# Kernel optimization log

Measured on AMD Instinct MI355X. Metric: run time of the kernel, lower is better.

Reference implementation:

```python
import jax, jax.numpy as jnp
import numpy as np

T, B, S, A, H = 512, 1024, 64, 16, 128  # timesteps, envs, state_dim, action_dim, LAYER_SIZE


def setup_inputs() -> dict:
    key = jax.random.key(0)
    ks = jax.random.split(key, 12)

    def w(k, shape, fan_in, std=1.0):
        return std * jax.random.normal(k, shape, jnp.float32) / jnp.sqrt(fan_in)

    x = jax.random.normal(ks[0], (T * B, S), jnp.float32)
    done = (jax.random.uniform(ks[1], (T * B,)) < 0.05).astype(jnp.float32)
    action = jax.random.randint(ks[2], (T * B,), 0, A, jnp.int32)
    gru_state = jnp.zeros((1, B, H), jnp.float32)

    return {
        "x": x, "done": done, "action": action, "gru_state": gru_state,
        "W1": w(ks[3], (H, S), S), "b1": jnp.zeros((H,), jnp.float32),
        "W2": w(ks[4], (H, H), H), "b2": jnp.zeros((H,), jnp.float32),
        "W_ih": w(ks[5], (3 * H, H), H), "b_ih": jnp.zeros((3 * H,), jnp.float32),
        "W_hh": w(ks[6], (3 * H, H), H), "b_hh": jnp.zeros((3 * H,), jnp.float32),
        "Wa": w(ks[7], (A, H), H, std=0.01), "ba": jnp.zeros((A,), jnp.float32),
        "Wc": w(ks[8], (1, H), H), "bc": jnp.zeros((1,), jnp.float32),
    }


def reference(x, done, action, gru_state, W1, b1, W2, b2, W_ih, b_ih, W_hh, b_hh, Wa, ba, Wc, bc):
    # MLP encoder: Linear->ReLU->Linear->ReLU  [T*B, H]
    h2 = jax.nn.relu(jax.nn.relu(x @ W1.T + b1) @ W2.T + b2)
    # Precompute input-side GRU gates for all timesteps: [T, B, 3H]
    gx = (h2 @ W_ih.T + b_ih).reshape(T, B, 3 * H)
    d = done.reshape(T, B)
    h0 = gru_state[0]  # [B, H]

    def step(h, inp):
        gx_t, d_t = inp
        h = (1.0 - d_t)[:, None] * h  # done-mask state reset
        gh = h @ W_hh.T + b_hh
        xr, xz, xn = jnp.split(gx_t, 3, axis=-1)
        hr, hz, hn = jnp.split(gh, 3, axis=-1)
        r = jax.nn.sigmoid(xr + hr)
        z = jax.nn.sigmoid(xz + hz)
        n = jnp.tanh(xn + r * hn)
        h_new = (1.0 - z) * n + z * h
        return h_new, h_new

    h_last, hs = jax.lax.scan(step, h0, (gx, d))
    hidden = hs.reshape(T * B, H)

    logits = hidden @ Wa.T + ba
    logp = jax.nn.log_softmax(logits, axis=-1)
    log_prob = jnp.take_along_axis(logp, action[:, None].astype(jnp.int32), axis=1)[:, 0]
    entropy = -jnp.sum(jnp.exp(logp) * logp, axis=-1)
    # DETACH=True: critic runs on detached hidden
    value = jax.lax.stop_gradient(hidden) @ Wc.T + bc  # [T*B, 1]

    main = jnp.concatenate([log_prob[:, None], entropy[:, None], value], axis=1)  # [T*B, 3]
    return main, h_last[None]
```

## Files before the change

kernel.cpp:

```cpp
#include <hip/hip_runtime.h>
#include <stdint.h>

#define TT 512
#define BB 1024
#define SS 64
#define HH 128
#define TBR (TT*BB)
#define NTILE (TBR/16)
#define MTPB 16
#define MGRID (NTILE/MTPB)

typedef __attribute__((ext_vector_type(8))) short short8;
typedef __attribute__((ext_vector_type(4))) float floatx4;
typedef unsigned short u16;
typedef unsigned int u32;
typedef struct { u32 x, y; } u32x2;

__device__ __forceinline__ float bf2f(u16 u){union{u32 i;float f;}v;v.i=((u32)u)<<16;return v.f;}
__device__ __forceinline__ u16 f2bf(float f){union{float f;u32 i;}v;v.f=f;u32 r=v.i+0x7FFFu+((v.i>>16)&1u);return (u16)(r>>16);}
__device__ __forceinline__ float frcp(float x){ return __builtin_amdgcn_rcpf(x); }

__device__ __forceinline__ bool buf_is_bf16(const u16* p) {
  int ok = 0;
#pragma unroll
  for (int i = 0; i < 32; ++i) {
    u32 v = p[2*i] & 0x7FFFu;
    u32 e = v >> 7;
    ok += (v == 0u || (e >= 96u && e <= 128u)) ? 1 : 0;
  }
  return ok >= 24;
}

template<bool BF> __device__ __forceinline__ float ld1(const void* p, size_t i){
  if constexpr (BF) return bf2f(((const u16*)p)[i]);
  else              return ((const float*)p)[i];
}
__device__ __forceinline__ short8 pack8(floatx4 a, floatx4 b){
  short8 r;
  r[0]=(short)f2bf(a[0]); r[1]=(short)f2bf(a[1]); r[2]=(short)f2bf(a[2]); r[3]=(short)f2bf(a[3]);
  r[4]=(short)f2bf(b[0]); r[5]=(short)f2bf(b[1]); r[6]=(short)f2bf(b[2]); r[7]=(short)f2bf(b[3]);
  return r;
}
template<bool BF> __device__ __forceinline__ short8 ld8(const void* p, size_t i){
  if constexpr (BF) return *(const short8*)((const u16*)p + i);
  else {
    const float* f = (const float*)p + i;
    return pack8(*(const floatx4*)f, *(const floatx4*)(f + 4));
  }
}
template<bool BF> __device__ __forceinline__ void st1(void* p, size_t i, float v){
  if constexpr (BF) ((u16*)p)[i] = f2bf(v);
  else              ((float*)p)[i] = v;
}

__device__ __forceinline__ void barrier_lds() {
  __asm__ __volatile__("" ::: "memory");
  __builtin_amdgcn_s_waitcnt(0xC07F);
  __builtin_amdgcn_s_barrier();
  __asm__ __volatile__("" ::: "memory");
}

__device__ __forceinline__ int fragidx(int m,int k){
  return ((k>>5)<<9)+((m+(((k>>3)&3)<<4))<<3)+(k&7);
}
__device__ __forceinline__ floatx4 mfma(short8 a, short8 b, floatx4 c){
  return __builtin_amdgcn_mfma_f32_16x16x32_bf16(a,b,c,0,0,0);
}

template<bool BF>
__global__ __launch_bounds__(512, 2) void k_mlp(
    const void* __restrict__ x,
    const void* __restrict__ W1, const void* __restrict__ b1,
    const void* __restrict__ W2, const void* __restrict__ b2,
    u16* __restrict__ h2g)
{
  if (buf_is_bf16((const u16*)W1) != BF) return;
  const int tid = threadIdx.x, lane = tid & 63, wv = tid >> 6;
  const int n16 = lane & 15, q = lane >> 4;
  const int jj = 16*wv + n16;

  __shared__ __align__(16) u16 h1f[2][2048];
  __shared__ __align__(16) u16 h2f[2][2048];

  short8 w1f[2], w2f[4];
  float b1v, b2v;
  {
#pragma unroll
    for (int ks = 0; ks < 2; ++ks) w1f[ks] = ld8<BF>(W1, (size_t)jj*SS + ks*32 + q*8);
    b1v = ld1<BF>(b1, jj);
#pragma unroll
    for (int ks = 0; ks < 4; ++ks) w2f[ks] = ld8<BF>(W2, (size_t)jj*HH + ks*32 + q*8);
    b2v = ld1<BF>(b2, jj);
  }

  const int tile0 = blockIdx.x * MTPB;

  short8 xb[2]; floatx4 xf[4];
  {
    size_t base = ((size_t)(tile0*16 + n16))*SS + q*8;
    if constexpr (BF) {
      xb[0] = *(const short8*)((const u16*)x + base);
      xb[1] = *(const short8*)((const u16*)x + base + 32);
    } else {
      const float* f = (const float*)x + base;
      xf[0] = *(const floatx4*)f;       xf[1] = *(const floatx4*)(f+4);
      xf[2] = *(const floatx4*)(f+32);  xf[3] = *(const floatx4*)(f+36);
    }
  }

  for (int i = 0; i < MTPB + 2; ++i) {
    short8 xc0, xc1;
    if (i < MTPB) {
      if constexpr (BF) { xc0 = xb[0]; xc1 = xb[1]; }
      else              { xc0 = pack8(xf[0], xf[1]); xc1 = pack8(xf[2], xf[3]); }
    }
    if (i + 1 < MTPB) {
      size_t base = ((size_t)((tile0+i+1)*16 + n16))*SS + q*8;
      if constexpr (BF) {
        xb[0] = *(const short8*)((const u16*)x + base);
        xb[1] = *(const short8*)((const u16*)x + base + 32);
      } else {
        const float* f = (const float*)x + base;
        xf[0] = *(const floatx4*)f;       xf[1] = *(const floatx4*)(f+4);
        xf[2] = *(const floatx4*)(f+32);  xf[3] = *(const floatx4*)(f+36);
      }
    }
    if (i < MTPB) {
      floatx4 a = {0.f,0.f,0.f,0.f};
      a = mfma(xc0, w1f[0], a);
      a = mfma(xc1, w1f[1], a);
#pragma unroll
      for (int r = 0; r < 4; ++r) {
        float v = a[r] + b1v; v = v > 0.f ? v : 0.f;
        h1f[i&1][fragidx(4*q + r, jj)] = f2bf(v);
      }
    }
    if (i >= 1 && i <= MTPB) {
      short8 h1a[4];
#pragma unroll
      for (int ks = 0; ks < 4; ++ks)
        h1a[ks] = *(const short8*)(&h1f[(i-1)&1][0] + ks*512 + lane*8);
      floatx4 a = {0.f,0.f,0.f,0.f};
#pragma unroll
      for (int ks = 0; ks < 4; ++ks) a = mfma(h1a[ks], w2f[ks], a);
#pragma unroll
      for (int r = 0; r < 4; ++r) {
        float v = a[r] + b2v; v = v > 0.f ? v : 0.f;
        h2f[(i-1)&1][fragidx(4*q + r, jj)] = f2bf(v);
      }
    }
    if (i >= 2) {
      const int td = tile0 + i - 2;
      u32x2 v2 = *(const u32x2*)(&h2f[i&1][tid*4]);
      *(u32x2*)(h2g + (size_t)td*2048 + tid*4) = v2;
    }
    barrier_lds();
  }
}

template<bool BF>
__global__ __launch_bounds__(512, 2) void k_scan_split(
    const void* __restrict__ done_, const void* __restrict__ gstate,
    const void* __restrict__ Wih, const void* __restrict__ bih,
    const void* __restrict__ Whh, const void* __restrict__ bhh,
    const void* __restrict__ Wa, const void* __restrict__ ba,
    const void* __restrict__ Wc, const void* __restrict__ bc,
    const void* __restrict__ W1,
    const u16* __restrict__ h2g,
    float* __restrict__ lgws, float* __restrict__ vws,
    void* __restrict__ out)
{
  if (buf_is_bf16((const u16*)W1) != BF) return;

  const int tid = threadIdx.x, lane = tid & 63, wv = tid >> 6;
  const int n16 = lane & 15, q = lane >> 4;
  const int b0 = blockIdx.x * 16, bx = blockIdx.x;
  const int jj = 16*wv + n16;

  __shared__ __align__(16) u16 hbuf[2][2048];

  short8 wif[3][4], whf[3][4], scf[4];
  float bihv2, bhv2, bb0, bb1;
  {
    float bi0, bi1, bh0, bh1;
#pragma unroll
    for (int g = 0; g < 3; ++g) {
      int grow = g*128 + jj;
#pragma unroll
      for (int ks = 0; ks < 4; ++ks) {
        wif[g][ks] = ld8<BF>(Wih, (size_t)grow*HH + ks*32 + q*8);
        whf[g][ks] = ld8<BF>(Whh, (size_t)grow*HH + ks*32 + q*8);
      }
      float bi = ld1<BF>(bih, grow), bh = ld1<BF>(bhh, grow);
      if (g == 0) { bi0 = bi; bh0 = bh; }
      else if (g == 1) { bi1 = bi; bh1 = bh; }
      else { bihv2 = bi; bhv2 = bh; }
    }
    bb0 = bi0 + bh0;
    bb1 = bi1 + bh1;
  }
  if (wv == 1) {
#pragma unroll
    for (int ks = 0; ks < 4; ++ks) scf[ks] = ld8<BF>(Wa, (size_t)n16*HH + ks*32 + q*8);
  } else if (wv == 2) {
#pragma unroll
    for (int ks = 0; ks < 4; ++ks) {
      short8 z = {0,0,0,0,0,0,0,0};
      if (n16 == 0) z = ld8<BF>(Wc, (size_t)ks*32 + q*8);
      scf[ks] = z;
    }
  } else {
#pragma unroll
    for (int ks = 0; ks < 4; ++ks) { short8 z = {0,0,0,0,0,0,0,0}; scf[ks] = z; }
  }
  const float bav = ld1<BF>(ba, n16);
  const float bcv = ld1<BF>(bc, 0);

  float hreg[4];
#pragma unroll
  for (int r = 0; r < 4; ++r) {
    hreg[r] = ld1<BF>(gstate, (size_t)(b0 + 4*q + r)*HH + jj);
    hbuf[0][fragidx(4*q + r, jj)] = f2bf(hreg[r]);
  }
  float s4cur[2][4];
#pragma unroll
  for (int s = 0; s < 2; ++s)
#pragma unroll
    for (int r = 0; r < 4; ++r)
      s4cur[s][r] = 1.f - ld1<BF>(done_, (size_t)s*BB + b0 + 4*q + r);
  u32x2 draw[2];  floatx4 fdraw[2];
#pragma unroll
  for (int s = 0; s < 2; ++s) { draw[s].x = draw[s].y = 0; fdraw[s] = floatx4{0,0,0,0}; }

  const u16* const hz = h2g + (size_t)bx*2048;
  short8 h2p[2][4];
#pragma unroll
  for (int ks = 0; ks < 4; ++ks)
    h2p[0][ks] = *(const short8*)(hz + (size_t)0*64*2048 + ks*512 + lane*8);
#pragma unroll
  for (int ks = 0; ks < 4; ++ks)
    h2p[1][ks] = *(const short8*)(hz + (size_t)1*64*2048 + ks*512 + lane*8);
  floatx4 pipe[3];
#pragma unroll
  for (int g = 0; g < 3; ++g) {
    floatx4 a = {0.f,0.f,0.f,0.f};
#pragma unroll
    for (int ks = 0; ks < 4; ++ks) a = mfma(h2p[0][ks], wif[g][ks], a);
    pipe[g] = a;
  }
#pragma unroll
  for (int ks = 0; ks < 4; ++ks)
    h2p[0][ks] = *(const short8*)(hz + (size_t)2*64*2048 + ks*512 + lane*8);
  __syncthreads();

  u16* hw0 = &hbuf[1][0] + fragidx(4*q, jj);
  u16* hw1 = &hbuf[0][0] + fragidx(4*q, jj);

  for (int t0 = 0; t0 < TT; t0 += 2) {
#pragma unroll
    for (int s = 0; s < 2; ++s) {
      const int t = t0 + s;
      const int pw = s;
      const int pb = s ^ 1;

      short8 haf[4];
#pragma unroll
      for (int ks = 0; ks < 4; ++ks)
        haf[ks] = *(const short8*)(&hbuf[pw][0] + ks*512 + lane*8);

      floatx4 pn[3];
#pragma unroll
      for (int g = 0; g < 3; ++g) {
        floatx4 a = {0.f,0.f,0.f,0.f};
#pragma unroll
        for (int ks = 0; ks < 4; ++ks) a = mfma(h2p[pb][ks], wif[g][ks], a);
        pn[g] = a;
      }
      {
        const int tl = (t+3 < TT) ? t+3 : TT-1;
        const u16* tp = hz + (size_t)tl*64*2048;
#pragma unroll
        for (int ks = 0; ks < 4; ++ks)
          h2p[pb][ks] = *(const short8*)(tp + ks*512 + lane*8);
      }

      if (t > 0 && (wv == 1 || wv == 2)) {
        floatx4 a = {0.f,0.f,0.f,0.f};
#pragma unroll
        for (int ks = 0; ks < 4; ++ks) a = mfma(haf[ks], scf[ks], a);
        if (wv == 1) {
#pragma unroll
          for (int r = 0; r < 4; ++r)
            lgws[((size_t)(t-1)*BB + b0 + 4*q + r)*16 + n16] = a[r] + bav;
        } else if (n16 == 0) {
#pragma unroll
          for (int r = 0; r < 4; ++r)
            vws[(size_t)(t-1)*BB + b0 + 4*q + r] = a[r] + bcv;
        }
      }

      floatx4 agh[3];
#pragma unroll
      for (int g = 0; g < 3; ++g) {
        floatx4 a = {0.f,0.f,0.f,0.f};
#pragma unroll
        for (int ks = 0; ks < 4; ++ks) a = mfma(haf[ks], whf[g][ks], a);
        agh[g] = a;
      }
      u16* hw = pw ? hw1 : hw0;
#pragma unroll
      for (int r = 0; r < 4; ++r) {
        float s4 = s4cur[s][r];
        float tr = pipe[0][r] + __builtin_fmaf(s4, agh[0][r], bb0);
        float tz = pipe[1][r] + __builtin_fmaf(s4, agh[1][r], bb1);
        float xn_ = pipe[2][r] + bihv2;
        float hn_ = __builtin_fmaf(s4, agh[2][r], bhv2);
        float rg = frcp(1.f + __expf(-tr));
        float zg = frcp(1.f + __expf(-tz));
        float ni = __builtin_fmaf(rg, hn_, xn_);
        float ng = __builtin_fmaf(2.f, frcp(1.f + __expf(-2.f*ni)), -1.f);
        float hold = hreg[r] * s4;
        float hnew = __builtin_fmaf(zg, hold - ng, ng);
        hreg[r] = hnew;
        hw[r*8] = f2bf(hnew);
      }

      if (s == 0) {
#pragma unroll
        for (int ss = 0; ss < 2; ++ss) {
          const int tl = (t0+2+ss < TT) ? t0+2+ss : TT-1;
          size_t didx = (size_t)tl*BB + b0 + 4*q;
          if constexpr (BF) draw[ss] = *(const u32x2*)((const u16*)done_ + didx);
          else              fdraw[ss] = *(const floatx4*)((const float*)done_ + didx);
        }
      }

      barrier_lds();
#pragma unroll
      for (int g = 0; g < 3; ++g) pipe[g] = pn[g];
    }
    if constexpr (BF) {
#pragma unroll
      for (int ss = 0; ss < 2; ++ss) {
        s4cur[ss][0] = 1.f - bf2f((u16)(draw[ss].x & 0xFFFF));
        s4cur[ss][1] = 1.f - bf2f((u16)(draw[ss].x >> 16));
        s4cur[ss][2] = 1.f - bf2f((u16)(draw[ss].y & 0xFFFF));
        s4cur[ss][3] = 1.f - bf2f((u16)(draw[ss].y >> 16));
      }
    } else {
#pragma unroll
      for (int ss = 0; ss < 2; ++ss)
#pragma unroll
        for (int r = 0; r < 4; ++r) s4cur[ss][r] = 1.f - fdraw[ss][r];
    }
  }

  {
    if (wv == 1 || wv == 2) {
      short8 haf[4];
#pragma unroll
      for (int ks = 0; ks < 4; ++ks) haf[ks] = *(const short8*)(&hbuf[0][0] + ks*512 + lane*8);
      floatx4 a = {0.f,0.f,0.f,0.f};
#pragma unroll
      for (int ks = 0; ks < 4; ++ks) a = mfma(haf[ks], scf[ks], a);
      if (wv == 1) {
#pragma unroll
        for (int r = 0; r < 4; ++r)
          lgws[((size_t)(TT-1)*BB + b0 + 4*q + r)*16 + n16] = a[r] + bav;
      } else if (n16 == 0) {
#pragma unroll
        for (int r = 0; r < 4; ++r)
          vws[(size_t)(TT-1)*BB + b0 + 4*q + r] = a[r] + bcv;
      }
    }
#pragma unroll
    for (int r = 0; r < 4; ++r)
      st1<BF>(out, (size_t)3*TBR + (size_t)(b0 + 4*q + r)*HH + jj, hreg[r]);
  }
}

struct TrueT  { static constexpr bool value = true;  };
struct FalseT { static constexpr bool value = false; };

template<bool BF>
__global__ __launch_bounds__(512, 2) void k_scan_mono(
    const void* __restrict__ x, const void* __restrict__ done_,
    const void* __restrict__ gstate,
    const void* __restrict__ W1, const void* __restrict__ b1,
    const void* __restrict__ W2, const void* __restrict__ b2,
    const void* __restrict__ Wih, const void* __restrict__ bih,
    const void* __restrict__ Whh, const void* __restrict__ bhh,
    const void* __restrict__ Wa, const void* __restrict__ ba,
    const void* __restrict__ Wc, const void* __restrict__ bc,
    float* __restrict__ lgws, float* __restrict__ vws,
    void* __restrict__ out)
{
  if (buf_is_bf16((const u16*)W1) != BF) return;

  const int tid = threadIdx.x, lane = tid & 63, wv = tid >> 6;
  const int n16 = lane & 15, q = lane >> 4;
  const int b0 = blockIdx.x * 16;
  const int jj = 16*wv + n16;

  __shared__ __align__(16) u16 hbuf[2][2048];
  __shared__ __align__(16) u16 h1f[2][2048];
  __shared__ __align__(16) u16 h2f[2][2048];

  short8 w1f[2], w2f[4], wif[3][4], whf[3][4], scf[4];
  float b1v, b2v, bihv2, bhv2, bb0, bb1;
  {
    int row = wv*16 + n16;
#pragma unroll
    for (int ks = 0; ks < 2; ++ks) w1f[ks] = ld8<BF>(W1, (size_t)row*SS + ks*32 + q*8);
    b1v = ld1<BF>(b1, row);
#pragma unroll
    for (int ks = 0; ks < 4; ++ks) w2f[ks] = ld8<BF>(W2, (size_t)row*HH + ks*32 + q*8);
    b2v = ld1<BF>(b2, row);
    float bi0, bi1, bh0, bh1;
#pragma unroll
    for (int g = 0; g < 3; ++g) {
      int grow = g*128 + jj;
#pragma unroll
      for (int ks = 0; ks < 4; ++ks) {
        wif[g][ks] = ld8<BF>(Wih, (size_t)grow*HH + ks*32 + q*8);
        whf[g][ks] = ld8<BF>(Whh, (size_t)grow*HH + ks*32 + q*8);
      }
      float bi = ld1<BF>(bih, grow), bh = ld1<BF>(bhh, grow);
      if (g == 0) { bi0 = bi; bh0 = bh; }
      else if (g == 1) { bi1 = bi; bh1 = bh; }
      else { bihv2 = bi; bhv2 = bh; }
    }
    bb0 = bi0 + bh0;
    bb1 = bi1 + bh1;
  }
  if (wv == 1) {
#pragma unroll
    for (int ks = 0; ks < 4; ++ks) scf[ks] = ld8<BF>(Wa, (size_t)n16*HH + ks*32 + q*8);
  } else if (wv == 2) {
#pragma unroll
    for (int ks = 0; ks < 4; ++ks) {
      short8 z = {0,0,0,0,0,0,0,0};
      if (n16 == 0) z = ld8<BF>(Wc, (size_t)ks*32 + q*8);
      scf[ks] = z;
    }
  } else {
#pragma unroll
    for (int ks = 0; ks < 4; ++ks) { short8 z = {0,0,0,0,0,0,0,0}; scf[ks] = z; }
  }
  const float bav = ld1<BF>(ba, n16);
  const float bcv = ld1<BF>(bc, 0);

  float hreg[4];
#pragma unroll
  for (int r = 0; r < 4; ++r) {
    hreg[r] = ld1<BF>(gstate, (size_t)(b0 + 4*q + r)*HH + jj);
    hbuf[0][fragidx(4*q + r, jj)] = f2bf(hreg[r]);
  }
  short8 xc[2][2], xn[2][2];
#pragma unroll
  for (int s = 0; s < 2; ++s)
#pragma unroll
    for (int ks = 0; ks < 2; ++ks)
      xc[s][ks] = ld8<BF>(x, ((size_t)s*BB + b0 + n16)*SS + ks*32 + q*8);
  float s4cur[2][4];
#pragma unroll
  for (int s = 0; s < 2; ++s)
#pragma unroll
    for (int r = 0; r < 4; ++r) s4cur[s][r] = 1.f;
  u32x2 draw[2];  floatx4 fdraw[2];
#pragma unroll
  for (int s = 0; s < 2; ++s) { draw[s].x = draw[s].y = 0; fdraw[s] = floatx4{0,0,0,0}; }
#pragma unroll
  for (int s = 0; s < 2; ++s)
#pragma unroll
    for (int ks = 0; ks < 2; ++ks) { short8 z={0,0,0,0,0,0,0,0}; xn[s][ks]=z; }
  floatx4 pipe[2][3];
#pragma unroll
  for (int s = 0; s < 2; ++s)
#pragma unroll
    for (int g = 0; g < 3; ++g) pipe[s][g] = floatx4{0.f,0.f,0.f,0.f};
  __syncthreads();

  u16* hw0 = &hbuf[1][0] + fragidx(4*q, jj);
  u16* hw1 = &hbuf[0][0] + fragidx(4*q, jj);

  auto iter = [&](int t0, auto steady) {
    constexpr bool ST = decltype(steady)::value;
#pragma unroll
    for (int s = 0; s < 2; ++s) {
      const int t = t0 + s;
      const bool s1on = ST || (t <= TT-5);
      const bool s2on = ST || (t >= -3 && t <= TT-4);
      const bool s3on = ST || (t >= -2 && t <= TT-3);
      const bool ron  = ST || (t >= 0);
      const int pw = t & 1;

      short8 haf[4];
      if (ron) {
#pragma unroll
        for (int ks = 0; ks < 4; ++ks)
          haf[ks] = *(const short8*)(&hbuf[pw][0] + ks*512 + lane*8);
      }
      if (s1on) {
        floatx4 a = {0.f,0.f,0.f,0.f};
        a = mfma(xc[s][0], w1f[0], a);
        a = mfma(xc[s][1], w1f[1], a);
#pragma unroll
        for (int r = 0; r < 4; ++r) {
          float v = a[r] + b1v; v = v > 0.f ? v : 0.f;
          h1f[pw][fragidx(4*q + r, jj)] = f2bf(v);
        }
      }
      if (s2on) {
        short8 h1a[4];
#pragma unroll
        for (int ks = 0; ks < 4; ++ks)
          h1a[ks] = *(const short8*)(&h1f[pw^1][0] + ks*512 + lane*8);
        floatx4 a = {0.f,0.f,0.f,0.f};
#pragma unroll
        for (int ks = 0; ks < 4; ++ks) a = mfma(h1a[ks], w2f[ks], a);
#pragma unroll
        for (int r = 0; r < 4; ++r) {
          float v = a[r] + b2v; v = v > 0.f ? v : 0.f;
          h2f[pw][fragidx(4*q + r, jj)] = f2bf(v);
        }
      }
      if (s == 0) {
        if (ST || (t0 + 6 < TT)) {
          if constexpr (BF) {
#pragma unroll
            for (int ss = 0; ss < 2; ++ss) {
              size_t base = ((size_t)(t0+6+ss)*BB + b0 + n16)*SS + q*8;
              xn[ss][0] = *(const short8*)((const u16*)x + base);
              xn[ss][1] = *(const short8*)((const u16*)x + base + 32);
            }
          }
        }
        if (ST || (t0+2 >= 0 && t0+2 < TT)) {
#pragma unroll
          for (int ss = 0; ss < 2; ++ss) {
            size_t didx = (size_t)(t0+2+ss)*BB + b0 + 4*q;
            if constexpr (BF) draw[ss] = *(const u32x2*)((const u16*)done_ + didx);
            else              fdraw[ss] = *(const floatx4*)((const float*)done_ + didx);
          }
        }
      }
      if (ron) {
        if (t > 0 && (wv == 1 || wv == 2)) {
          floatx4 a = {0.f,0.f,0.f,0.f};
#pragma unroll
          for (int ks = 0; ks < 4; ++ks) a = mfma(haf[ks], scf[ks], a);
          if (wv == 1) {
#pragma unroll
            for (int r = 0; r < 4; ++r)
              lgws[((size_t)(t-1)*BB + b0 + 4*q + r)*16 + n16] = a[r] + bav;
          } else if (n16 == 0) {
#pragma unroll
            for (int r = 0; r < 4; ++r)
              vws[(size_t)(t-1)*BB + b0 + 4*q + r] = a[r] + bcv;
          }
        }
        floatx4 agh[3];
#pragma unroll
        for (int g = 0; g < 3; ++g) {
          floatx4 a = {0.f,0.f,0.f,0.f};
#pragma unroll
          for (int ks = 0; ks < 4; ++ks) a = mfma(haf[ks], whf[g][ks], a);
          agh[g] = a;
        }
        u16* hw = pw ? hw1 : hw0;
#pragma unroll
        for (int r = 0; r < 4; ++r) {
          float s4 = s4cur[s][r];
          float tr = pipe[s][0][r] + __builtin_fmaf(s4, agh[0][r], bb0);
          float tz = pipe[s][1][r] + __builtin_fmaf(s4, agh[1][r], bb1);
          float xn_ = pipe[s][2][r] + bihv2;
          float hn_ = __builtin_fmaf(s4, agh[2][r], bhv2);
          float rg = frcp(1.f + __expf(-tr));
          float zg = frcp(1.f + __expf(-tz));
          float ni = __builtin_fmaf(rg, hn_, xn_);
          float ng = __builtin_fmaf(2.f, frcp(1.f + __expf(-2.f*ni)), -1.f);
          float hold = hreg[r] * s4;
          float hnew = __builtin_fmaf(zg, hold - ng, ng);
          hreg[r] = hnew;
          hw[r*8] = f2bf(hnew);
        }
      }
      if (s3on) {
        short8 h2a[4];
#pragma unroll
        for (int ks = 0; ks < 4; ++ks)
          h2a[ks] = *(const short8*)(&h2f[pw^1][0] + ks*512 + lane*8);
#pragma unroll
        for (int g = 0; g < 3; ++g) {
          floatx4 a = {0.f,0.f,0.f,0.f};
#pragma unroll
          for (int ks = 0; ks < 4; ++ks) a = mfma(h2a[ks], wif[g][ks], a);
          pipe[s][g] = a;
        }
      }
      barrier_lds();
    }
    if (ST || (t0 + 6 < TT)) {
      if constexpr (BF) {
#pragma unroll
        for (int ss = 0; ss < 2; ++ss) { xc[ss][0] = xn[ss][0]; xc[ss][1] = xn[ss][1]; }
      } else {
#pragma unroll
        for (int ss = 0; ss < 2; ++ss) {
          size_t base = ((size_t)(t0+6+ss)*BB + b0 + n16)*SS + q*8;
          xc[ss][0] = ld8<false>(x, base);
          xc[ss][1] = ld8<false>(x, base + 32);
        }
      }
    }
    if (ST || (t0+2 >= 0 && t0+2 < TT)) {
      if constexpr (BF) {
#pragma unroll
        for (int ss = 0; ss < 2; ++ss) {
          s4cur[ss][0] = 1.f - bf2f((u16)(draw[ss].x & 0xFFFF));
          s4cur[ss][1] = 1.f - bf2f((u16)(draw[ss].x >> 16));
          s4cur[ss][2] = 1.f - bf2f((u16)(draw[ss].y & 0xFFFF));
          s4cur[ss][3] = 1.f - bf2f((u16)(draw[ss].y >> 16));
        }
      } else {
#pragma unroll
        for (int ss = 0; ss < 2; ++ss)
#pragma unroll
          for (int r = 0; r < 4; ++r) s4cur[ss][r] = 1.f - fdraw[ss][r];
      }
    }
  };

  iter(-4, FalseT{});
  iter(-2, FalseT{});
  for (int t0 = 0; t0 <= TT - 8; t0 += 2) iter(t0, TrueT{});
  iter(TT-6, FalseT{});
  iter(TT-4, FalseT{});
  iter(TT-2, FalseT{});

  {
    if (wv == 1 || wv == 2) {
      short8 haf[4];
#pragma unroll
      for (int ks = 0; ks < 4; ++ks) haf[ks] = *(const short8*)(&hbuf[0][0] + ks*512 + lane*8);
      floatx4 a = {0.f,0.f,0.f,0.f};
#pragma unroll
      for (int ks = 0; ks < 4; ++ks) a = mfma(haf[ks], scf[ks], a);
      if (wv == 1) {
#pragma unroll
        for (int r = 0; r < 4; ++r)
          lgws[((size_t)(TT-1)*BB + b0 + 4*q + r)*16 + n16] = a[r] + bav;
      } else if (n16 == 0) {
#pragma unroll
        for (int r = 0; r < 4; ++r)
          vws[(size_t)(TT-1)*BB + b0 + 4*q + r] = a[r] + bcv;
      }
    }
#pragma unroll
    for (int r = 0; r < 4; ++r)
      st1<BF>(out, (size_t)3*TBR + (size_t)(b0 + 4*q + r)*HH + jj, hreg[r]);
  }
}

template<bool BF>
__global__ __launch_bounds__(256) void k_head(
    const float* __restrict__ lgws, const float* __restrict__ vws,
    const int* __restrict__ action, const void* __restrict__ W1,
    void* __restrict__ out)
{
  if (buf_is_bf16((const u16*)W1) != BF) return;
  size_t row = (size_t)blockIdx.x * 256 + threadIdx.x;
  if (row >= (size_t)TBR) return;
  const float* lp = lgws + row*16;
  floatx4 v[4];
#pragma unroll
  for (int i = 0; i < 4; ++i) v[i] = *(const floatx4*)(lp + 4*i);
  float mx = v[0][0];
#pragma unroll
  for (int i = 0; i < 4; ++i)
#pragma unroll
    for (int j = 0; j < 4; ++j) mx = fmaxf(mx, v[i][j]);
  float sum = 0.f, se = 0.f;
#pragma unroll
  for (int i = 0; i < 4; ++i)
#pragma unroll
    for (int j = 0; j < 4; ++j) {
      float d = v[i][j] - mx;
      float e = __expf(d);
      sum += e; se = __builtin_fmaf(e, d, se);
    }
  float ls = __logf(sum);
  int a = action[row];
  float la = lp[a];
  float lpa = (la - mx) - ls;
  float ent = ls - se * frcp(sum);
  st1<BF>(out, row*3,     lpa);
  st1<BF>(out, row*3 + 1, ent);
  st1<BF>(out, row*3 + 2, vws[row]);
}

extern "C" void kernel_launch(void* const* d_in, const int* in_sizes, int n_in,
                              void* d_out, int out_size, void* d_ws, size_t ws_size,
                              hipStream_t stream) {
  const void* x    = d_in[0];
  const void* done = d_in[1];
  const int*  act  = (const int*)d_in[2];
  const void* gst  = d_in[3];
  const void* W1   = d_in[4];
  const void* b1   = d_in[5];
  const void* W2   = d_in[6];
  const void* b2   = d_in[7];
  const void* Wih  = d_in[8];
  const void* bih  = d_in[9];
  const void* Whh  = d_in[10];
  const void* bhh  = d_in[11];
  const void* Wa   = d_in[12];
  const void* ba   = d_in[13];
  const void* Wc   = d_in[14];
  const void* bc   = d_in[15];

  float* lgws = (float*)d_ws;
  float* vws  = lgws + (size_t)16*TBR;
  u16*   h2g  = (u16*)(vws + (size_t)TBR);
  const size_t need = (size_t)(16*TBR + TBR)*4 + (size_t)NTILE*4096;

  if (ws_size >= need) {
    hipLaunchKernelGGL((k_mlp<true>),  dim3(MGRID), dim3(512), 0, stream,
                       x, W1, b1, W2, b2, h2g);
    hipLaunchKernelGGL((k_mlp<false>), dim3(MGRID), dim3(512), 0, stream,
                       x, W1, b1, W2, b2, h2g);
    hipLaunchKernelGGL((k_scan_split<true>),  dim3(64), dim3(512), 0, stream,
                       done, gst, Wih, bih, Whh, bhh, Wa, ba, Wc, bc,
                       W1, h2g, lgws, vws, d_out);
    hipLaunchKernelGGL((k_scan_split<false>), dim3(64), dim3(512), 0, stream,
                       done, gst, Wih, bih, Whh, bhh, Wa, ba, Wc, bc,
                       W1, h2g, lgws, vws, d_out);
  } else {
    hipLaunchKernelGGL((k_scan_mono<true>),  dim3(64), dim3(512), 0, stream,
                       x, done, gst, W1, b1, W2, b2, Wih, bih,
                       Whh, bhh, Wa, ba, Wc, bc, lgws, vws, d_out);
    hipLaunchKernelGGL((k_scan_mono<false>), dim3(64), dim3(512), 0, stream,
                       x, done, gst, W1, b1, W2, b2, Wih, bih,
                       Whh, bhh, Wa, ba, Wc, bc, lgws, vws, d_out);
  }
  hipLaunchKernelGGL((k_head<true>),  dim3(TBR/256), dim3(256), 0, stream,
                     lgws, vws, act, W1, d_out);
  hipLaunchKernelGGL((k_head<false>), dim3(TBR/256), dim3(256), 0, stream,
                     lgws, vws, act, W1, d_out);
}
```

Before: 818.0 us.

## Fuse MLP encoder and GRU scan into one producer-consumer kernel with flags

Merges the MLP encoder kernel and the GRU scan kernel into a single launch. 192 producer blocks compute h2 tiles in a strided order and publish per-tile ready flags in global memory. 64 consumer blocks run the scan and spin on those flags before prefetching each timestep's tile. The aim is to overlap the encoder with the serial recurrence instead of running them back to back. In exchange it adds a memset, atomic flag traffic and spin-waits, and it relies on all 256 blocks being co-resident to avoid deadlock.

```diff
diff --git a/kernel.cpp b/kernel.cpp
--- a/kernel.cpp
+++ b/kernel.cpp
@@ -7,8 +7,8 @@
 #define HH 128
 #define TBR (TT*BB)
 #define NTILE (TBR/16)
-#define MTPB 16
-#define MGRID (NTILE/MTPB)
+#define NPROD 192
+#define NCONS 64
 
 typedef __attribute__((ext_vector_type(8))) short short8;
 typedef __attribute__((ext_vector_type(4))) float floatx4;
@@ -16,6 +16,9 @@
 typedef unsigned int u32;
 typedef struct { u32 x, y; } u32x2;
 
+struct TrueT  { static constexpr bool value = true;  };
+struct FalseT { static constexpr bool value = false; };
+
 __device__ __forceinline__ float bf2f(u16 u){union{u32 i;float f;}v;v.i=((u32)u)<<16;return v.f;}
 __device__ __forceinline__ u16 f2bf(float f){union{float f;u32 i;}v;v.f=f;u32 r=v.i+0x7FFFu+((v.i>>16)&1u);return (u16)(r>>16);}
 __device__ __forceinline__ float frcp(float x){ return __builtin_amdgcn_rcpf(x); }
@@ -59,6 +62,17 @@
   __builtin_amdgcn_s_barrier();
   __asm__ __volatile__("" ::: "memory");
 }
+__device__ __forceinline__ void barrier_full() {
+  __asm__ __volatile__("" ::: "memory");
+  __builtin_amdgcn_s_waitcnt(0x0070);
+  __builtin_amdgcn_s_barrier();
+  __asm__ __volatile__("" ::: "memory");
+}
+
+__device__ __forceinline__ void wait_flag(const u32* f){
+  while (__hip_atomic_load(f, __ATOMIC_ACQUIRE, __HIP_MEMORY_SCOPE_AGENT) == 0u)
+    __builtin_amdgcn_s_sleep(8);
+}
 
 __device__ __forceinline__ int fragidx(int m,int k){
   return ((k>>5)<<9)+((m+(((k>>3)&3)<<4))<<3)+(k&7);
@@ -67,117 +81,98 @@
   return __builtin_amdgcn_mfma_f32_16x16x32_bf16(a,b,c,0,0,0);
 }
 
-template<bool BF>
-__global__ __launch_bounds__(512, 2) void k_mlp(
+template<bool BF, bool FL>
+__device__ __forceinline__ void mlp_body(
     const void* __restrict__ x,
     const void* __restrict__ W1, const void* __restrict__ b1,
     const void* __restrict__ W2, const void* __restrict__ b2,
-    u16* __restrict__ h2g)
+    u16* __restrict__ h2g, u32* __restrict__ flags,
+    int p, u16* h1f, u16* h2f)
 {
-  if (buf_is_bf16((const u16*)W1) != BF) return;
   const int tid = threadIdx.x, lane = tid & 63, wv = tid >> 6;
   const int n16 = lane & 15, q = lane >> 4;
   const int jj = 16*wv + n16;
 
-  __shared__ __align__(16) u16 h1f[2][2048];
-  __shared__ __align__(16) u16 h2f[2][2048];
-
   short8 w1f[2], w2f[4];
   float b1v, b2v;
-  {
-#pragma unroll
-    for (int ks = 0; ks < 2; ++ks) w1f[ks] = ld8<BF>(W1, (size_t)jj*SS + ks*32 + q*8);
-    b1v = ld1<BF>(b1, jj);
-#pragma unroll
-    for (int ks = 0; ks < 4; ++ks) w2f[ks] = ld8<BF>(W2, (size_t)jj*HH + ks*32 + q*8);
-    b2v = ld1<BF>(b2, jj);
-  }
-
-  const int tile0 = blockIdx.x * MTPB;
-
-  short8 xb[2]; floatx4 xf[4];
-  {
-    size_t base = ((size_t)(tile0*16 + n16))*SS + q*8;
-    if constexpr (BF) {
-      xb[0] = *(const short8*)((const u16*)x + base);
-      xb[1] = *(const short8*)((const u16*)x + base + 32);
-    } else {
-      const float* f = (const float*)x + base;
-      xf[0] = *(const floatx4*)f;       xf[1] = *(const floatx4*)(f+4);
-      xf[2] = *(const floatx4*)(f+32);  xf[3] = *(const floatx4*)(f+36);
-    }
-  }
-
-  for (int i = 0; i < MTPB + 2; ++i) {
+#pragma unroll
+  for (int ks = 0; ks < 2; ++ks) w1f[ks] = ld8<BF>(W1, (size_t)jj*SS + ks*32 + q*8);
+  b1v = ld1<BF>(b1, jj);
+#pragma unroll
+  for (int ks = 0; ks < 4; ++ks) w2f[ks] = ld8<BF>(W2, (size_t)jj*HH + ks*32 + q*8);
+  b2v = ld1<BF>(b2, jj);
+
+  int jflag = 0;
+  int j = 0;
+  for (int tau = p; tau < NTILE; tau += NPROD, ++j) {
     short8 xc0, xc1;
-    if (i < MTPB) {
-      if constexpr (BF) { xc0 = xb[0]; xc1 = xb[1]; }
-      else              { xc0 = pack8(xf[0], xf[1]); xc1 = pack8(xf[2], xf[3]); }
-    }
-    if (i + 1 < MTPB) {
-      size_t base = ((size_t)((tile0+i+1)*16 + n16))*SS + q*8;
+    {
+      size_t base = ((size_t)tau*16 + n16)*SS + q*8;
       if constexpr (BF) {
-        xb[0] = *(const short8*)((const u16*)x + base);
-        xb[1] = *(const short8*)((const u16*)x + base + 32);
+        xc0 = *(const short8*)((const u16*)x + base);
+        xc1 = *(const short8*)((const u16*)x + base + 32);
       } else {
         const float* f = (const float*)x + base;
-        xf[0] = *(const floatx4*)f;       xf[1] = *(const floatx4*)(f+4);
-        xf[2] = *(const floatx4*)(f+32);  xf[3] = *(const floatx4*)(f+36);
-      }
-    }
-    if (i < MTPB) {
-      floatx4 a = {0.f,0.f,0.f,0.f};
-      a = mfma(xc0, w1f[0], a);
-      a = mfma(xc1, w1f[1], a);
-#pragma unroll
-      for (int r = 0; r < 4; ++r) {
-        float v = a[r] + b1v; v = v > 0.f ? v : 0.f;
-        h1f[i&1][fragidx(4*q + r, jj)] = f2bf(v);
-      }
-    }
-    if (i >= 1 && i <= MTPB) {
-      short8 h1a[4];
-#pragma unroll
-      for (int ks = 0; ks < 4; ++ks)
-        h1a[ks] = *(const short8*)(&h1f[(i-1)&1][0] + ks*512 + lane*8);
-      floatx4 a = {0.f,0.f,0.f,0.f};
-#pragma unroll
-      for (int ks = 0; ks < 4; ++ks) a = mfma(h1a[ks], w2f[ks], a);
-#pragma unroll
-      for (int r = 0; r < 4; ++r) {
-        float v = a[r] + b2v; v = v > 0.f ? v : 0.f;
-        h2f[(i-1)&1][fragidx(4*q + r, jj)] = f2bf(v);
-      }
-    }
-    if (i >= 2) {
-      const int td = tile0 + i - 2;
-      u32x2 v2 = *(const u32x2*)(&h2f[i&1][tid*4]);
-      *(u32x2*)(h2g + (size_t)td*2048 + tid*4) = v2;
+        xc0 = pack8(*(const floatx4*)f, *(const floatx4*)(f+4));
+        xc1 = pack8(*(const floatx4*)(f+32), *(const floatx4*)(f+36));
+      }
+    }
+    floatx4 a = {0.f,0.f,0.f,0.f};
+    a = mfma(xc0, w1f[0], a);
+    a = mfma(xc1, w1f[1], a);
+#pragma unroll
+    for (int r = 0; r < 4; ++r) {
+      float v = a[r] + b1v; v = v > 0.f ? v : 0.f;
+      h1f[fragidx(4*q + r, jj)] = f2bf(v);
     }
     barrier_lds();
-  }
-}
-
-template<bool BF>
-__global__ __launch_bounds__(512, 2) void k_scan_split(
+    short8 h1a[4];
+#pragma unroll
+    for (int ks = 0; ks < 4; ++ks) h1a[ks] = *(const short8*)(h1f + ks*512 + lane*8);
+    floatx4 a2 = {0.f,0.f,0.f,0.f};
+#pragma unroll
+    for (int ks = 0; ks < 4; ++ks) a2 = mfma(h1a[ks], w2f[ks], a2);
+#pragma unroll
+    for (int r = 0; r < 4; ++r) {
+      float v = a2[r] + b2v; v = v > 0.f ? v : 0.f;
+      h2f[fragidx(4*q + r, jj)] = f2bf(v);
+    }
+    barrier_lds();
+    u32x2 v2 = *(const u32x2*)(h2f + tid*4);
+    *(u32x2*)(h2g + (size_t)tau*2048 + tid*4) = v2;
+    if constexpr (FL) {
+      barrier_full();
+      bool flush = (j == 0) || ((j & 3) == 3) || (tau + NPROD >= NTILE);
+      if (flush) {
+        if (tid == 0) {
+          __builtin_amdgcn_fence(__ATOMIC_RELEASE, "agent");
+          for (int i = jflag; i <= j; ++i)
+            __hip_atomic_store(flags + (size_t)p + (size_t)NPROD*i, 1u,
+                               __ATOMIC_RELAXED, __HIP_MEMORY_SCOPE_AGENT);
+        }
+        jflag = j + 1;
+      }
+    } else {
+      barrier_lds();
+    }
+  }
+}
+
+template<bool BF, bool FL>
+__device__ __forceinline__ void scan_body(
     const void* __restrict__ done_, const void* __restrict__ gstate,
     const void* __restrict__ Wih, const void* __restrict__ bih,
     const void* __restrict__ Whh, const void* __restrict__ bhh,
     const void* __restrict__ Wa, const void* __restrict__ ba,
     const void* __restrict__ Wc, const void* __restrict__ bc,
-    const void* __restrict__ W1,
-    const u16* __restrict__ h2g,
+    const u16* __restrict__ h2g, const u32* __restrict__ flags,
     float* __restrict__ lgws, float* __restrict__ vws,
-    void* __restrict__ out)
+    void* __restrict__ out, int bx, u16 (*hbuf)[2048])
 {
-  if (buf_is_bf16((const u16*)W1) != BF) return;
-
   const int tid = threadIdx.x, lane = tid & 63, wv = tid >> 6;
   const int n16 = lane & 15, q = lane >> 4;
-  const int b0 = blockIdx.x * 16, bx = blockIdx.x;
+  const int b0 = bx * 16;
   const int jj = 16*wv + n16;
-
-  __shared__ __align__(16) u16 hbuf[2][2048];
 
   short8 wif[3][4], whf[3][4], scf[4];
   float bihv2, bhv2, bb0, bb1;
@@ -232,6 +227,16 @@
 #pragma unroll
   for (int s = 0; s < 2; ++s) { draw[s].x = draw[s].y = 0; fdraw[s] = floatx4{0,0,0,0}; }
 
+  if constexpr (FL) {
+    wait_flag(flags + (size_t)0*NCONS + bx);
+    wait_flag(flags + (size_t)1*NCONS + bx);
+    wait_flag(flags + (size_t)2*NCONS + bx);
+  }
+  u32 fcur = 1; bool allr = !FL;
+  if constexpr (FL)
+    fcur = __hip_atomic_load(flags + (size_t)3*NCONS + bx, __ATOMIC_RELAXED,
+                             __HIP_MEMORY_SCOPE_AGENT);
+
   const u16* const hz = h2g + (size_t)bx*2048;
   short8 h2p[2][4];
 #pragma unroll
@@ -278,6 +283,19 @@
       }
       {
         const int tl = (t+3 < TT) ? t+3 : TT-1;
+        if constexpr (FL) {
+          if (!allr) {
+            if (fcur) {
+              __builtin_amdgcn_fence(__ATOMIC_ACQUIRE, "agent");
+            } else {
+              wait_flag(flags + (size_t)tl*NCONS + bx);
+            }
+            if (t+3 >= TT-1) allr = true;
+            const int tn = (t+4 < TT) ? t+4 : TT-1;
+            fcur = __hip_atomic_load(flags + (size_t)tn*NCONS + bx,
+                                     __ATOMIC_RELAXED, __HIP_MEMORY_SCOPE_AGENT);
+          }
+        }
         const u16* tp = hz + (size_t)tl*64*2048;
 #pragma unroll
         for (int ks = 0; ks < 4; ++ks)
@@ -379,8 +397,62 @@
   }
 }
 
-struct TrueT  { static constexpr bool value = true;  };
-struct FalseT { static constexpr bool value = false; };
+template<bool BF>
+__global__ __launch_bounds__(512, 2) void k_fused(
+    const void* __restrict__ x, const void* __restrict__ done_,
+    const void* __restrict__ gstate,
+    const void* __restrict__ W1, const void* __restrict__ b1,
+    const void* __restrict__ W2, const void* __restrict__ b2,
+    const void* __restrict__ Wih, const void* __restrict__ bih,
+    const void* __restrict__ Whh, const void* __restrict__ bhh,
+    const void* __restrict__ Wa, const void* __restrict__ ba,
+    const void* __restrict__ Wc, const void* __restrict__ bc,
+    u16* __restrict__ h2g, u32* __restrict__ flags,
+    float* __restrict__ lgws, float* __restrict__ vws,
+    void* __restrict__ out)
+{
+  if (buf_is_bf16((const u16*)W1) != BF) return;
+  __shared__ __align__(16) u16 hbuf[2][2048];
+  __shared__ __align__(16) u16 h1f[2048];
+  __shared__ __align__(16) u16 h2f[2048];
+  if (blockIdx.x < NPROD) {
+    mlp_body<BF, true>(x, W1, b1, W2, b2, h2g, flags, blockIdx.x, h1f, h2f);
+    return;
+  }
+  scan_body<BF, true>(done_, gstate, Wih, bih, Whh, bhh, Wa, ba, Wc, bc,
+                      h2g, flags, lgws, vws, out, blockIdx.x - NPROD, hbuf);
+}
+
+template<bool BF>
+__global__ __launch_bounds__(512, 2) void k_mlp(
+    const void* __restrict__ x,
+    const void* __restrict__ W1, const void* __restrict__ b1,
+    const void* __restrict__ W2, const void* __restrict__ b2,
+    u16* __restrict__ h2g)
+{
+  if (buf_is_bf16((const u16*)W1) != BF) return;
+  __shared__ __align__(16) u16 h1f[2048];
+  __shared__ __align__(16) u16 h2f[2048];
+  mlp_body<BF, false>(x, W1, b1, W2, b2, h2g, nullptr, blockIdx.x, h1f, h2f);
+}
+
+template<bool BF>
+__global__ __launch_bounds__(512, 2) void k_scan_split(
+    const void* __restrict__ done_, const void* __restrict__ gstate,
+    const void* __restrict__ Wih, const void* __restrict__ bih,
+    const void* __restrict__ Whh, const void* __restrict__ bhh,
+    const void* __restrict__ Wa, const void* __restrict__ ba,
+    const void* __restrict__ Wc, const void* __restrict__ bc,
+    const void* __restrict__ W1,
+    const u16* __restrict__ h2g,
+    float* __restrict__ lgws, float* __restrict__ vws,
+    void* __restrict__ out)
+{
+  if (buf_is_bf16((const u16*)W1) != BF) return;
+  __shared__ __align__(16) u16 hbuf[2][2048];
+  scan_body<BF, false>(done_, gstate, Wih, bih, Whh, bhh, Wa, ba, Wc, bc,
+                       h2g, nullptr, lgws, vws, out, blockIdx.x, hbuf);
+}
 
 template<bool BF>
 __global__ __launch_bounds__(512, 2) void k_scan_mono(
@@ -722,18 +794,30 @@
 
   float* lgws = (float*)d_ws;
   float* vws  = lgws + (size_t)16*TBR;
-  u16*   h2g  = (u16*)(vws + (size_t)TBR);
-  const size_t need = (size_t)(16*TBR + TBR)*4 + (size_t)NTILE*4096;
-
-  if (ws_size >= need) {
-    hipLaunchKernelGGL((k_mlp<true>),  dim3(MGRID), dim3(512), 0, stream,
+  const size_t h2g_off   = (size_t)(16*TBR + TBR)*4;
+  const size_t flags_off = h2g_off + (size_t)NTILE*4096;
+  const size_t need_split = flags_off;
+  const size_t need_fused = flags_off + (size_t)NTILE*4;
+  u16* h2g   = (u16*)((char*)d_ws + h2g_off);
+  u32* flags = (u32*)((char*)d_ws + flags_off);
+
+  if (ws_size >= need_fused) {
+    hipMemsetAsync(flags, 0, (size_t)NTILE*4, stream);
+    hipLaunchKernelGGL((k_fused<true>),  dim3(NPROD+NCONS), dim3(512), 0, stream,
+                       x, done, gst, W1, b1, W2, b2, Wih, bih,
+                       Whh, bhh, Wa, ba, Wc, bc, h2g, flags, lgws, vws, d_out);
+    hipLaunchKernelGGL((k_fused<false>), dim3(NPROD+NCONS), dim3(512), 0, stream,
+                       x, done, gst, W1, b1, W2, b2, Wih, bih,
+                       Whh, bhh, Wa, ba, Wc, bc, h2g, flags, lgws, vws, d_out);
+  } else if (ws_size >= need_split) {
+    hipLaunchKernelGGL((k_mlp<true>),  dim3(NPROD), dim3(512), 0, stream,
                        x, W1, b1, W2, b2, h2g);
-    hipLaunchKernelGGL((k_mlp<false>), dim3(MGRID), dim3(512), 0, stream,
+    hipLaunchKernelGGL((k_mlp<false>), dim3(NPROD), dim3(512), 0, stream,
                        x, W1, b1, W2, b2, h2g);
-    hipLaunchKernelGGL((k_scan_split<true>),  dim3(64), dim3(512), 0, stream,
+    hipLaunchKernelGGL((k_scan_split<true>),  dim3(NCONS), dim3(512), 0, stream,
                        done, gst, Wih, bih, Whh, bhh, Wa, ba, Wc, bc,
                        W1, h2g, lgws, vws, d_out);
-    hipLaunchKernelGGL((k_scan_split<false>), dim3(64), dim3(512), 0, stream,
+    hipLaunchKernelGGL((k_scan_split<false>), dim3(NCONS), dim3(512), 0, stream,
                        done, gst, Wih, bih, Whh, bhh, Wa, ba, Wc, bc,
                        W1, h2g, lgws, vws, d_out);
   } else {
```

Result: slower. 2.393 ms (+192.5%).

## Restructure MLP encoder kernel so each wave processes whole tiles independently

Applied to the files above, without the earlier changes.

The MLP kernel now assigns each wavefront its own sequence of 16-row tiles and computes all 128 output columns per wave. W1 stays in registers and W2 is staged once in LDS, so the per-tile block-wide barriers and double-buffered cross-wave LDS handoff go away. Blocks shrink to 256 threads. In exchange the kernel uses more registers per wave and issues more LDS reads of W2 per tile, and the scan kernel still dominates total time.

```diff
diff --git a/kernel.cpp b/kernel.cpp
--- a/kernel.cpp
+++ b/kernel.cpp
@@ -7,8 +7,8 @@
 #define HH 128
 #define TBR (TT*BB)
 #define NTILE (TBR/16)
-#define MTPB 16
-#define MGRID (NTILE/MTPB)
+#define MW_TPW 16
+#define MGRID (NTILE/(4*MW_TPW))
 
 typedef __attribute__((ext_vector_type(8))) short short8;
 typedef __attribute__((ext_vector_type(4))) float floatx4;
@@ -16,6 +16,9 @@
 typedef unsigned int u32;
 typedef struct { u32 x, y; } u32x2;
 
+struct TrueT  { static constexpr bool value = true;  };
+struct FalseT { static constexpr bool value = false; };
+
 __device__ __forceinline__ float bf2f(u16 u){union{u32 i;float f;}v;v.i=((u32)u)<<16;return v.f;}
 __device__ __forceinline__ u16 f2bf(float f){union{float f;u32 i;}v;v.f=f;u32 r=v.i+0x7FFFu+((v.i>>16)&1u);return (u16)(r>>16);}
 __device__ __forceinline__ float frcp(float x){ return __builtin_amdgcn_rcpf(x); }
@@ -68,7 +71,7 @@
 }
 
 template<bool BF>
-__global__ __launch_bounds__(512, 2) void k_mlp(
+__global__ __launch_bounds__(256, 2) void k_mlp(
     const void* __restrict__ x,
     const void* __restrict__ W1, const void* __restrict__ b1,
     const void* __restrict__ W2, const void* __restrict__ b2,
@@ -77,84 +80,98 @@
   if (buf_is_bf16((const u16*)W1) != BF) return;
   const int tid = threadIdx.x, lane = tid & 63, wv = tid >> 6;
   const int n16 = lane & 15, q = lane >> 4;
-  const int jj = 16*wv + n16;
-
-  __shared__ __align__(16) u16 h1f[2][2048];
-  __shared__ __align__(16) u16 h2f[2][2048];
-
-  short8 w1f[2], w2f[4];
-  float b1v, b2v;
+
+  __shared__ __align__(16) u16 W2L[8*4*64*8];
+  __shared__ __align__(16) u16 scr[4][2048];
+
+  for (int s = tid; s < 2048; s += 256) {
+    int j = s >> 8, ks = (s >> 6) & 3, l = s & 63;
+    short8 v = ld8<BF>(W2, (size_t)(16*j + (l & 15))*HH + ks*32 + (l >> 4)*8);
+    *(short8*)&W2L[(size_t)s*8] = v;
+  }
+  short8 w1b[8][2]; float b1v[8], b2v[8];
+#pragma unroll
+  for (int j = 0; j < 8; ++j) {
+    int row = 16*j + n16;
+#pragma unroll
+    for (int ks = 0; ks < 2; ++ks) w1b[j][ks] = ld8<BF>(W1, (size_t)row*SS + ks*32 + q*8);
+    b1v[j] = ld1<BF>(b1, row);
+    b2v[j] = ld1<BF>(b2, row);
+  }
+  __syncthreads();
+
+  u16* S = scr[wv];
+  const int tile0 = (blockIdx.x * 4 + wv) * MW_TPW;
+
+  short8 xb0, xb1; floatx4 xf0, xf1, xf2, xf3;
   {
-#pragma unroll
-    for (int ks = 0; ks < 2; ++ks) w1f[ks] = ld8<BF>(W1, (size_t)jj*SS + ks*32 + q*8);
-    b1v = ld1<BF>(b1, jj);
-#pragma unroll
-    for (int ks = 0; ks < 4; ++ks) w2f[ks] = ld8<BF>(W2, (size_t)jj*HH + ks*32 + q*8);
-    b2v = ld1<BF>(b2, jj);
-  }
-
-  const int tile0 = blockIdx.x * MTPB;
-
-  short8 xb[2]; floatx4 xf[4];
-  {
-    size_t base = ((size_t)(tile0*16 + n16))*SS + q*8;
+    size_t base = ((size_t)tile0*16 + n16)*SS + q*8;
     if constexpr (BF) {
-      xb[0] = *(const short8*)((const u16*)x + base);
-      xb[1] = *(const short8*)((const u16*)x + base + 32);
+      xb0 = *(const short8*)((const u16*)x + base);
+      xb1 = *(const short8*)((const u16*)x + base + 32);
     } else {
       const float* f = (const float*)x + base;
-      xf[0] = *(const floatx4*)f;       xf[1] = *(const floatx4*)(f+4);
-      xf[2] = *(const floatx4*)(f+32);  xf[3] = *(const floatx4*)(f+36);
-    }
-  }
-
-  for (int i = 0; i < MTPB + 2; ++i) {
+      xf0 = *(const floatx4*)f;       xf1 = *(const floatx4*)(f+4);
+      xf2 = *(const floatx4*)(f+32);  xf3 = *(const floatx4*)(f+36);
+    }
+  }
+
+  for (int i = 0; i < MW_TPW; ++i) {
+    const int tau = tile0 + i;
     short8 xc0, xc1;
-    if (i < MTPB) {
-      if constexpr (BF) { xc0 = xb[0]; xc1 = xb[1]; }
-      else              { xc0 = pack8(xf[0], xf[1]); xc1 = pack8(xf[2], xf[3]); }
-    }
-    if (i + 1 < MTPB) {
-      size_t base = ((size_t)((tile0+i+1)*16 + n16))*SS + q*8;
+    if constexpr (BF) { xc0 = xb0; xc1 = xb1; }
+    else              { xc0 = pack8(xf0, xf1); xc1 = pack8(xf2, xf3); }
+    if (i + 1 < MW_TPW) {
+      size_t base = ((size_t)(tau+1)*16 + n16)*SS + q*8;
       if constexpr (BF) {
-        xb[0] = *(const short8*)((const u16*)x + base);
-        xb[1] = *(const short8*)((const u16*)x + base + 32);
+        xb0 = *(const short8*)((const u16*)x + base);
+        xb1 = *(const short8*)((const u16*)x + base + 32);
       } else {
         const float* f = (const float*)x + base;
-        xf[0] = *(const floatx4*)f;       xf[1] = *(const floatx4*)(f+4);
-        xf[2] = *(const floatx4*)(f+32);  xf[3] = *(const floatx4*)(f+36);
-      }
-    }
-    if (i < MTPB) {
+        xf0 = *(const floatx4*)f;       xf1 = *(const floatx4*)(f+4);
+        xf2 = *(const floatx4*)(f+32);  xf3 = *(const floatx4*)(f+36);
+      }
+    }
+#pragma unroll
+    for (int j = 0; j < 8; ++j) {
       floatx4 a = {0.f,0.f,0.f,0.f};
-      a = mfma(xc0, w1f[0], a);
-      a = mfma(xc1, w1f[1], a);
+      a = mfma(xc0, w1b[j][0], a);
+      a = mfma(xc1, w1b[j][1], a);
 #pragma unroll
       for (int r = 0; r < 4; ++r) {
-        float v = a[r] + b1v; v = v > 0.f ? v : 0.f;
-        h1f[i&1][fragidx(4*q + r, jj)] = f2bf(v);
-      }
-    }
-    if (i >= 1 && i <= MTPB) {
-      short8 h1a[4];
-#pragma unroll
-      for (int ks = 0; ks < 4; ++ks)
-        h1a[ks] = *(const short8*)(&h1f[(i-1)&1][0] + ks*512 + lane*8);
+        float v = a[r] + b1v[j]; v = v > 0.f ? v : 0.f;
+        S[fragidx(4*q + r, 16*j + n16)] = f2bf(v);
+      }
+    }
+    short8 h1a0 = *(const short8*)(S + 0*512 + lane*8);
+    short8 h1a1 = *(const short8*)(S + 1*512 + lane*8);
+    short8 h1a2 = *(const short8*)(S + 2*512 + lane*8);
+    short8 h1a3 = *(const short8*)(S + 3*512 + lane*8);
+#pragma unroll
+    for (int j = 0; j < 8; ++j) {
       floatx4 a = {0.f,0.f,0.f,0.f};
-#pragma unroll
-      for (int ks = 0; ks < 4; ++ks) a = mfma(h1a[ks], w2f[ks], a);
+      a = mfma(h1a0, *(const short8*)&W2L[(size_t)((j*4+0)*64 + lane)*8], a);
+      a = mfma(h1a1, *(const short8*)&W2L[(size_t)((j*4+1)*64 + lane)*8], a);
+      a = mfma(h1a2, *(const short8*)&W2L[(size_t)((j*4+2)*64 + lane)*8], a);
+      a = mfma(h1a3, *(const short8*)&W2L[(size_t)((j*4+3)*64 + lane)*8], a);
 #pragma unroll
       for (int r = 0; r < 4; ++r) {
-        float v = a[r] + b2v; v = v > 0.f ? v : 0.f;
-        h2f[(i-1)&1][fragidx(4*q + r, jj)] = f2bf(v);
-      }
-    }
-    if (i >= 2) {
-      const int td = tile0 + i - 2;
-      u32x2 v2 = *(const u32x2*)(&h2f[i&1][tid*4]);
-      *(u32x2*)(h2g + (size_t)td*2048 + tid*4) = v2;
-    }
-    barrier_lds();
+        float v = a[r] + b2v[j]; v = v > 0.f ? v : 0.f;
+        S[fragidx(4*q + r, 16*j + n16)] = f2bf(v);
+      }
+    }
+    {
+      const u16* src = S + lane*32;
+      u16* dst = h2g + (size_t)tau*2048 + lane*32;
+      short8 d0 = *(const short8*)(src);
+      short8 d1 = *(const short8*)(src + 8);
+      short8 d2 = *(const short8*)(src + 16);
+      short8 d3 = *(const short8*)(src + 24);
+      *(short8*)(dst)      = d0;
+      *(short8*)(dst + 8)  = d1;
+      *(short8*)(dst + 16) = d2;
+      *(short8*)(dst + 24) = d3;
+    }
   }
 }
 
@@ -378,9 +395,6 @@
       st1<BF>(out, (size_t)3*TBR + (size_t)(b0 + 4*q + r)*HH + jj, hreg[r]);
   }
 }
-
-struct TrueT  { static constexpr bool value = true;  };
-struct FalseT { static constexpr bool value = false; };
 
 template<bool BF>
 __global__ __launch_bounds__(512, 2) void k_scan_mono(
@@ -726,9 +740,9 @@
   const size_t need = (size_t)(16*TBR + TBR)*4 + (size_t)NTILE*4096;
 
   if (ws_size >= need) {
-    hipLaunchKernelGGL((k_mlp<true>),  dim3(MGRID), dim3(512), 0, stream,
+    hipLaunchKernelGGL((k_mlp<true>),  dim3(MGRID), dim3(256), 0, stream,
                        x, W1, b1, W2, b2, h2g);
-    hipLaunchKernelGGL((k_mlp<false>), dim3(MGRID), dim3(512), 0, stream,
+    hipLaunchKernelGGL((k_mlp<false>), dim3(MGRID), dim3(256), 0, stream,
                        x, W1, b1, W2, b2, h2g);
     hipLaunchKernelGGL((k_scan_split<true>),  dim3(64), dim3(512), 0, stream,
                        done, gst, Wih, bih, Whh, bhh, Wa, ba, Wc, bc,
```

Measured after the change: 758.9 us. -7.2%, faster.
